# Kernel optimization log

Measured on AMD Instinct MI355X. Metric: run time of the kernel, lower is better.

The kernel has to match this reference:

```python
import jax, jax.numpy as jnp
import numpy as np

B, M, L, D, S = 2, 4, 1024, 256, 16
WSCALE = 0.02  # keep exp(delta*A) well-conditioned

def setup_inputs() -> dict:
    key = jax.random.key(0)
    ks = jax.random.split(key, 6)
    x = jax.random.normal(ks[0], (B, M, L, D), dtype=jnp.float32)
    v = jax.random.normal(ks[1], (B, M, L, D), dtype=jnp.float32)
    W1 = jax.random.normal(ks[2], (D, D), dtype=jnp.float32) * WSCALE
    W2 = jax.random.normal(ks[3], (D, S), dtype=jnp.float32) * WSCALE
    W3 = jax.random.normal(ks[4], (D, S), dtype=jnp.float32) * WSCALE
    A = jax.random.normal(ks[5], (D, S), dtype=jnp.float32) * WSCALE
    b1 = jnp.zeros((D,), jnp.float32)
    b2 = jnp.zeros((S,), jnp.float32)
    b3 = jnp.zeros((S,), jnp.float32)
    h = jnp.zeros((B, L, M, D, S), jnp.float32)
    return {"x": x, "v": v, "W1": W1, "b1": b1, "W2": W2, "b2": b2,
            "W3": W3, "b3": b3, "A": A, "h": h}

def reference(x, v, W1, b1, W2, b2, W3, b3, A, h):
    Bb, Mm, Ll, Dd = x.shape
    Ss = W2.shape[1]
    # projections on flattened (B*M*L, D), then reshaped to (B, L, M, .)
    # NOTE: this reinterprets the (M, L) flattening order, matching the
    # original torch code's .view(-1, D) followed by .view(B, L, M, .).
    xf = x.reshape(-1, Dd)
    vf = v.reshape(-1, Dd)
    E  = (vf @ W2 + b2).reshape(Bb, Ll, Mm, Ss)
    Bm = (xf @ W2 + b2).reshape(Bb, Ll, Mm, Ss)
    C  = (xf @ W3 + b3).reshape(Bb, Ll, Mm, Ss)
    x_fc1 = xf @ W1 + b1
    Dm = x_fc1.reshape(Bb, Ll, Mm, Dd)
    Fm = (vf @ W1 + b1).reshape(Bb, Ll, Mm, Dd)
    delta = jax.nn.softplus(x_fc1).reshape(Bb, Ll, Mm, Dd)
    # discretization: dB/dE outer products, dA = exp(delta * A)
    dB = delta[..., :, None] * Bm[..., None, :]          # (B,L,M,D,S)
    dE = delta[..., :, None] * E[..., None, :]           # (B,L,M,D,S)
    dA = jnp.exp(jnp.einsum('blmd,dn->blmdn', delta, A)) # (B,L,M,D,S)
    # state update (h is a zeros buffer in the original, never carried)
    xt = jnp.transpose(x, (0, 2, 1, 3))  # (B,L,M,D)
    vt = jnp.transpose(v, (0, 2, 1, 3))
    h_new = dA * h + xt[..., None] * dB + vt[..., None] * dE
    y = jnp.einsum('blmn,blmdn->blmd', C, h_new)
    return y * Dm + y * Fm + y
```

## Files before the change

### kernel.cpp

```cpp
#include <hip/hip_runtime.h>
#include <cmath>


#define DD 256

typedef __bf16 bf16x8 __attribute__((ext_vector_type(8)));
typedef float  f32x4  __attribute__((ext_vector_type(4)));
typedef unsigned short us8 __attribute__((ext_vector_type(8)));

static __device__ __forceinline__ float softplus_f(float x) {
    return fmaxf(x, 0.0f) + log1pf(expf(-fabsf(x)));
}

__global__ void prep_w(const float* __restrict__ W1, const float* __restrict__ W2,
                       const float* __restrict__ W3, unsigned short* __restrict__ WT)
{
    const int b = blockIdx.x, tid = threadIdx.x;
    if (b < 64) {
        __shared__ float t[32][33];
        const int ti = b >> 3, tj = b & 7;
        #pragma unroll
        for (int it = 0; it < 4; ++it) {
            const int idx = it * 256 + tid;
            const int r = idx >> 5, c = idx & 31;
            t[r][c] = W1[(size_t)(ti * 32 + r) * 256 + tj * 32 + c];
        }
        __syncthreads();
        #pragma unroll
        for (int it = 0; it < 4; ++it) {
            const int idx = it * 256 + tid;
            const int rr = idx >> 5, cc = idx & 31;
            const __bf16 h = (__bf16)t[cc][rr];
            WT[(size_t)(tj * 32 + rr) * 256 + ti * 32 + cc] =
                __builtin_bit_cast(unsigned short, h);
        }
    } else {
        const int w = b - 64;
        const float* __restrict__ W = w ? W3 : W2;
        for (int e = tid; e < 4096; e += 256) {
            const int s = e >> 8, k = e & 255;
            const __bf16 h = (__bf16)W[k * 16 + s];
            WT[(size_t)(256 + w * 16 + s) * 256 + k] =
                __builtin_bit_cast(unsigned short, h);
        }
    }
}

__global__ __launch_bounds__(256, 2) void s6_main(
    const float* __restrict__ x, const float* __restrict__ v,
    const unsigned short* __restrict__ WT,
    const float* __restrict__ b1, const float* __restrict__ b2,
    const float* __restrict__ b3, float* __restrict__ out)
{
    const int wv   = threadIdx.x >> 6;
    const int lane = threadIdx.x & 63;
    const int ar   = lane & 15;
    const int g    = lane >> 4;
    const int q0   = blockIdx.x * 16;
    const int T0   = wv * 4;

    bf16x8 ax[8], av[8];
    #pragma unroll
    for (int ks = 0; ks < 8; ++ks) {
        const size_t base = (size_t)(q0 + ar) * DD + ks * 32 + g * 8;
        const float4 x0 = *(const float4*)(x + base);
        const float4 x1 = *(const float4*)(x + base + 4);
        const float4 v0 = *(const float4*)(v + base);
        const float4 v1 = *(const float4*)(v + base + 4);
        bf16x8 a, b;
        a[0] = (__bf16)x0.x; a[1] = (__bf16)x0.y; a[2] = (__bf16)x0.z; a[3] = (__bf16)x0.w;
        a[4] = (__bf16)x1.x; a[5] = (__bf16)x1.y; a[6] = (__bf16)x1.z; a[7] = (__bf16)x1.w;
        b[0] = (__bf16)v0.x; b[1] = (__bf16)v0.y; b[2] = (__bf16)v0.z; b[3] = (__bf16)v0.w;
        b[4] = (__bf16)v1.x; b[5] = (__bf16)v1.y; b[6] = (__bf16)v1.z; b[7] = (__bf16)v1.w;
        ax[ks] = a; av[ks] = b;
    }

    f32x4 aX[4], aV[4];
    f32x4 aBm = {0.f,0.f,0.f,0.f}, aE = {0.f,0.f,0.f,0.f}, aC = {0.f,0.f,0.f,0.f};
    #pragma unroll
    for (int i = 0; i < 4; ++i) {
        aX[i] = (f32x4){0.f,0.f,0.f,0.f};
        aV[i] = (f32x4){0.f,0.f,0.f,0.f};
    }

    #pragma unroll
    for (int ks = 0; ks < 8; ++ks) {
        const int ko = ks * 32 + g * 8;
        #pragma unroll
        for (int i = 0; i < 4; ++i) {
            const int n = (T0 + i) * 16 + ar;
            const us8 bw = *(const us8*)(WT + (size_t)n * DD + ko);
            const bf16x8 bf = __builtin_bit_cast(bf16x8, bw);
            aX[i] = __builtin_amdgcn_mfma_f32_16x16x32_bf16(ax[ks], bf, aX[i], 0, 0, 0);
            aV[i] = __builtin_amdgcn_mfma_f32_16x16x32_bf16(av[ks], bf, aV[i], 0, 0, 0);
        }
        {
            const us8 bw2 = *(const us8*)(WT + (size_t)(256 + ar) * DD + ko);
            const bf16x8 bf2 = __builtin_bit_cast(bf16x8, bw2);
            aBm = __builtin_amdgcn_mfma_f32_16x16x32_bf16(ax[ks], bf2, aBm, 0, 0, 0);
            aE  = __builtin_amdgcn_mfma_f32_16x16x32_bf16(av[ks], bf2, aE , 0, 0, 0);
            const us8 bw3 = *(const us8*)(WT + (size_t)(272 + ar) * DD + ko);
            const bf16x8 bf3 = __builtin_bit_cast(bf16x8, bw3);
            aC  = __builtin_amdgcn_mfma_f32_16x16x32_bf16(ax[ks], bf3, aC , 0, 0, 0);
        }
    }

    float s1j[4], s2j[4];
    {
        const float bb2 = b2[ar];
        const float bb3 = b3[ar];
        #pragma unroll
        for (int j = 0; j < 4; ++j) {
            const float C = aC[j] + bb3;
            float pb = C * (aBm[j] + bb2);
            float pe = C * (aE[j]  + bb2);
            #pragma unroll
            for (int off = 8; off >= 1; off >>= 1) {
                pb += __shfl_xor(pb, off);
                pe += __shfl_xor(pe, off);
            }
            s1j[j] = pb; s2j[j] = pe;
        }
    }

    #pragma unroll
    for (int i = 0; i < 4; ++i) {
        const int d = (T0 + i) * 16 + ar;
        const float bb1 = b1[d];
        #pragma unroll
        for (int j = 0; j < 4; ++j) {
            const int row = g * 4 + j;
            const int q = q0 + row;
            const float p1 = aX[i][j] + bb1;
            const float pv = aV[i][j] + bb1;
            const int bq = q >> 12, fq = q & 4095, li = fq >> 2, m = fq & 3;
            const size_t rp = ((size_t)(bq << 12) + (m << 10) + li) * DD + d;
            const float xt = x[rp];
            const float vt = v[rp];
            const float dl = softplus_f(p1);
            const float y  = dl * (xt * s1j[j] + vt * s2j[j]);
            out[(size_t)q * DD + d] = y * (1.0f + p1 + pv);
        }
    }
}

extern "C" void kernel_launch(void* const* d_in, const int* in_sizes, int n_in,
                              void* d_out, int out_size, void* d_ws, size_t ws_size,
                              hipStream_t stream) {
    const float* x  = (const float*)d_in[0];
    const float* v  = (const float*)d_in[1];
    const float* W1 = (const float*)d_in[2];
    const float* b1 = (const float*)d_in[3];
    const float* W2 = (const float*)d_in[4];
    const float* b2 = (const float*)d_in[5];
    const float* W3 = (const float*)d_in[6];
    const float* b3 = (const float*)d_in[7];
    float* out = (float*)d_out;
    unsigned short* WT = (unsigned short*)d_ws;

    hipLaunchKernelGGL(prep_w, dim3(66), dim3(256), 0, stream, W1, W2, W3, WT);
    hipLaunchKernelGGL(s6_main, dim3(512), dim3(256), 0, stream,
                       x, v, WT, b1, b2, b3, out);
}
```

Measured before the change: 217.3 us.

## Pre-swizzle weights into MFMA fragment order and split columns over eight waves

The weight prep kernel now writes W1/W2/W3 as bf16 in the exact per-lane MFMA B-fragment order, so the main kernel reads each fragment as one contiguous 16-byte load per lane. The main kernel moves to 512 threads per block with each wave owning two 16-column tiles instead of four, and no longer holds all eight A fragments in registers; x/v are converted per k-step inside the loop. The aim is coalesced weight loads, lower register pressure and more waves per CU. In exchange every wave reloads and reconverts the same x/v row tile and recomputes the shared Bm/E/C projections, doubling that redundant work across the block.

Result: no change. 214.2 us (-1.5%).

```diff
diff --git a/kernel.cpp b/kernel.cpp
--- a/kernel.cpp
+++ b/kernel.cpp
@@ -13,53 +13,52 @@
 }
 
 __global__ void prep_w(const float* __restrict__ W1, const float* __restrict__ W2,
-                       const float* __restrict__ W3, unsigned short* __restrict__ WT)
+                       const float* __restrict__ W3, unsigned short* __restrict__ WTf)
 {
-    const int b = blockIdx.x, tid = threadIdx.x;
-    if (b < 64) {
-        __shared__ float t[32][33];
-        const int ti = b >> 3, tj = b & 7;
+    const int tid  = blockIdx.x * 256 + threadIdx.x;
+    const int lane = tid & 63;
+    const int ks   = (tid >> 6) & 7;
+    const int t    = tid >> 9;
+    const int k0   = ks * 32 + (lane >> 4) * 8;
+    const int nl   = lane & 15;
+    unsigned short o[8];
+    if (t < 16) {
+        const int n = t * 16 + nl;
         #pragma unroll
-        for (int it = 0; it < 4; ++it) {
-            const int idx = it * 256 + tid;
-            const int r = idx >> 5, c = idx & 31;
-            t[r][c] = W1[(size_t)(ti * 32 + r) * 256 + tj * 32 + c];
-        }
-        __syncthreads();
-        #pragma unroll
-        for (int it = 0; it < 4; ++it) {
-            const int idx = it * 256 + tid;
-            const int rr = idx >> 5, cc = idx & 31;
-            const __bf16 h = (__bf16)t[cc][rr];
-            WT[(size_t)(tj * 32 + rr) * 256 + ti * 32 + cc] =
-                __builtin_bit_cast(unsigned short, h);
+        for (int j = 0; j < 8; ++j) {
+            const __bf16 h = (__bf16)W1[(size_t)(k0 + j) * 256 + n];
+            o[j] = __builtin_bit_cast(unsigned short, h);
         }
     } else {
-        const int w = b - 64;
-        const float* __restrict__ W = w ? W3 : W2;
-        for (int e = tid; e < 4096; e += 256) {
-            const int s = e >> 8, k = e & 255;
-            const __bf16 h = (__bf16)W[k * 16 + s];
-            WT[(size_t)(256 + w * 16 + s) * 256 + k] =
-                __builtin_bit_cast(unsigned short, h);
+        const float* __restrict__ W = (t == 16) ? W2 : W3;
+        #pragma unroll
+        for (int j = 0; j < 8; ++j) {
+            const __bf16 h = (__bf16)W[(size_t)(k0 + j) * 16 + nl];
+            o[j] = __builtin_bit_cast(unsigned short, h);
         }
     }
+    *(us8*)(WTf + (size_t)tid * 8) = *(const us8*)o;
 }
 
-__global__ __launch_bounds__(256, 2) void s6_main(
+__global__ __launch_bounds__(512, 4) void s6_main(
     const float* __restrict__ x, const float* __restrict__ v,
-    const unsigned short* __restrict__ WT,
+    const unsigned short* __restrict__ WTf,
     const float* __restrict__ b1, const float* __restrict__ b2,
     const float* __restrict__ b3, float* __restrict__ out)
 {
-    const int wv   = threadIdx.x >> 6;
+    const int w    = threadIdx.x >> 6;
     const int lane = threadIdx.x & 63;
     const int ar   = lane & 15;
     const int g    = lane >> 4;
     const int q0   = blockIdx.x * 16;
-    const int T0   = wv * 4;
+    const int T0   = w * 2;
 
-    bf16x8 ax[8], av[8];
+    f32x4 aX0 = {0.f,0.f,0.f,0.f}, aX1 = {0.f,0.f,0.f,0.f};
+    f32x4 aV0 = {0.f,0.f,0.f,0.f}, aV1 = {0.f,0.f,0.f,0.f};
+    f32x4 aBm = {0.f,0.f,0.f,0.f}, aE  = {0.f,0.f,0.f,0.f}, aC = {0.f,0.f,0.f,0.f};
+
+    const us8* __restrict__ fb = (const us8*)WTf;
+
     #pragma unroll
     for (int ks = 0; ks < 8; ++ks) {
         const size_t base = (size_t)(q0 + ar) * DD + ks * 32 + g * 8;
@@ -67,42 +66,24 @@
         const float4 x1 = *(const float4*)(x + base + 4);
         const float4 v0 = *(const float4*)(v + base);
         const float4 v1 = *(const float4*)(v + base + 4);
-        bf16x8 a, b;
-        a[0] = (__bf16)x0.x; a[1] = (__bf16)x0.y; a[2] = (__bf16)x0.z; a[3] = (__bf16)x0.w;
-        a[4] = (__bf16)x1.x; a[5] = (__bf16)x1.y; a[6] = (__bf16)x1.z; a[7] = (__bf16)x1.w;
-        b[0] = (__bf16)v0.x; b[1] = (__bf16)v0.y; b[2] = (__bf16)v0.z; b[3] = (__bf16)v0.w;
-        b[4] = (__bf16)v1.x; b[5] = (__bf16)v1.y; b[6] = (__bf16)v1.z; b[7] = (__bf16)v1.w;
-        ax[ks] = a; av[ks] = b;
-    }
+        bf16x8 axk, avk;
+        axk[0] = (__bf16)x0.x; axk[1] = (__bf16)x0.y; axk[2] = (__bf16)x0.z; axk[3] = (__bf16)x0.w;
+        axk[4] = (__bf16)x1.x; axk[5] = (__bf16)x1.y; axk[6] = (__bf16)x1.z; axk[7] = (__bf16)x1.w;
+        avk[0] = (__bf16)v0.x; avk[1] = (__bf16)v0.y; avk[2] = (__bf16)v0.z; avk[3] = (__bf16)v0.w;
+        avk[4] = (__bf16)v1.x; avk[5] = (__bf16)v1.y; avk[6] = (__bf16)v1.z; avk[7] = (__bf16)v1.w;
 
-    f32x4 aX[4], aV[4];
-    f32x4 aBm = {0.f,0.f,0.f,0.f}, aE = {0.f,0.f,0.f,0.f}, aC = {0.f,0.f,0.f,0.f};
-    #pragma unroll
-    for (int i = 0; i < 4; ++i) {
-        aX[i] = (f32x4){0.f,0.f,0.f,0.f};
-        aV[i] = (f32x4){0.f,0.f,0.f,0.f};
-    }
+        const bf16x8 bf0 = __builtin_bit_cast(bf16x8, fb[((T0 + 0) * 8 + ks) * 64 + lane]);
+        const bf16x8 bf1 = __builtin_bit_cast(bf16x8, fb[((T0 + 1) * 8 + ks) * 64 + lane]);
+        const bf16x8 bf2 = __builtin_bit_cast(bf16x8, fb[(16 * 8 + ks) * 64 + lane]);
+        const bf16x8 bf3 = __builtin_bit_cast(bf16x8, fb[(17 * 8 + ks) * 64 + lane]);
 
-    #pragma unroll
-    for (int ks = 0; ks < 8; ++ks) {
-        const int ko = ks * 32 + g * 8;
-        #pragma unroll
-        for (int i = 0; i < 4; ++i) {
-            const int n = (T0 + i) * 16 + ar;
-            const us8 bw = *(const us8*)(WT + (size_t)n * DD + ko);
-            const bf16x8 bf = __builtin_bit_cast(bf16x8, bw);
-            aX[i] = __builtin_amdgcn_mfma_f32_16x16x32_bf16(ax[ks], bf, aX[i], 0, 0, 0);
-            aV[i] = __builtin_amdgcn_mfma_f32_16x16x32_bf16(av[ks], bf, aV[i], 0, 0, 0);
-        }
-        {
-            const us8 bw2 = *(const us8*)(WT + (size_t)(256 + ar) * DD + ko);
-            const bf16x8 bf2 = __builtin_bit_cast(bf16x8, bw2);
-            aBm = __builtin_amdgcn_mfma_f32_16x16x32_bf16(ax[ks], bf2, aBm, 0, 0, 0);
-            aE  = __builtin_amdgcn_mfma_f32_16x16x32_bf16(av[ks], bf2, aE , 0, 0, 0);
-            const us8 bw3 = *(const us8*)(WT + (size_t)(272 + ar) * DD + ko);
-            const bf16x8 bf3 = __builtin_bit_cast(bf16x8, bw3);
-            aC  = __builtin_amdgcn_mfma_f32_16x16x32_bf16(ax[ks], bf3, aC , 0, 0, 0);
-        }
+        aX0 = __builtin_amdgcn_mfma_f32_16x16x32_bf16(axk, bf0, aX0, 0, 0, 0);
+        aV0 = __builtin_amdgcn_mfma_f32_16x16x32_bf16(avk, bf0, aV0, 0, 0, 0);
+        aX1 = __builtin_amdgcn_mfma_f32_16x16x32_bf16(axk, bf1, aX1, 0, 0, 0);
+        aV1 = __builtin_amdgcn_mfma_f32_16x16x32_bf16(avk, bf1, aV1, 0, 0, 0);
+        aBm = __builtin_amdgcn_mfma_f32_16x16x32_bf16(axk, bf2, aBm, 0, 0, 0);
+        aE  = __builtin_amdgcn_mfma_f32_16x16x32_bf16(avk, bf2, aE , 0, 0, 0);
+        aC  = __builtin_amdgcn_mfma_f32_16x16x32_bf16(axk, bf3, aC , 0, 0, 0);
     }
 
     float s1j[4], s2j[4];
@@ -124,15 +105,17 @@
     }
 
     #pragma unroll
-    for (int i = 0; i < 4; ++i) {
+    for (int i = 0; i < 2; ++i) {
+        const f32x4& AX = i ? aX1 : aX0;
+        const f32x4& AV = i ? aV1 : aV0;
         const int d = (T0 + i) * 16 + ar;
         const float bb1 = b1[d];
         #pragma unroll
         for (int j = 0; j < 4; ++j) {
             const int row = g * 4 + j;
             const int q = q0 + row;
-            const float p1 = aX[i][j] + bb1;
-            const float pv = aV[i][j] + bb1;
+            const float p1 = AX[j] + bb1;
+            const float pv = AV[j] + bb1;
             const int bq = q >> 12, fq = q & 4095, li = fq >> 2, m = fq & 3;
             const size_t rp = ((size_t)(bq << 12) + (m << 10) + li) * DD + d;
             const float xt = x[rp];
@@ -156,9 +139,9 @@
     const float* W3 = (const float*)d_in[6];
     const float* b3 = (const float*)d_in[7];
     float* out = (float*)d_out;
-    unsigned short* WT = (unsigned short*)d_ws;
+    unsigned short* WTf = (unsigned short*)d_ws;
 
-    hipLaunchKernelGGL(prep_w, dim3(66), dim3(256), 0, stream, W1, W2, W3, WT);
-    hipLaunchKernelGGL(s6_main, dim3(512), dim3(256), 0, stream,
-                       x, v, WT, b1, b2, b3, out);
+    hipLaunchKernelGGL(prep_w, dim3(36), dim3(256), 0, stream, W1, W2, W3, WTf);
+    hipLaunchKernelGGL(s6_main, dim3(512), dim3(512), 0, stream,
+                       x, v, WTf, b1, b2, b3, out);
 }
```
